# Optimization experiments

Hardware: AMD Instinct MI355X
Metric: run time of the kernel (lower is better)

## Reference

```python
import jax, jax.numpy as jnp
import numpy as np

N_NODE = 100000
N_EDGE = 1600000
D_FEAT = 64
DEPTH = 3
BASEALPHA = 1.0


def setup_inputs() -> dict:
    key = jax.random.key(0)
    k1, k2, k3 = jax.random.split(key, 3)
    x = jax.random.normal(k1, (N_NODE, D_FEAT), dtype=jnp.float32)
    edge_index = jax.random.randint(k2, (2, N_EDGE), 0, N_NODE, dtype=jnp.int64)
    edge_attr = jax.random.uniform(k3, (N_EDGE,), dtype=jnp.float32)
    # learnable polynomial coefficients, init = min(1/alpha, 1) = 1.0
    alphas = jnp.ones((DEPTH + 1,), dtype=jnp.float32)
    return {"x": x, "edge_index": edge_index, "edge_attr": edge_attr, "alphas": alphas}


def reference(x, edge_index, edge_attr, alphas):
    n = x.shape[0]
    row, col = edge_index[0], edge_index[1]
    # GCN symmetric degree normalization: val_e = d_row^-1/2 * w_e * d_col^-1/2
    deg = jax.ops.segment_sum(edge_attr, row, num_segments=n)
    safe_deg = jnp.where(deg > 0, deg, 1.0)
    dinv = jnp.where(deg > 0, jax.lax.rsqrt(safe_deg), 0.0)
    val = dinv[row] * edge_attr * dinv[col]  # [E]

    a = BASEALPHA * jnp.tanh(alphas)  # [depth+1]

    def spmm(h):  # (adj @ h): out[i] = sum_{e: row_e=i} val_e * h[col_e]
        return jax.ops.segment_sum(val[:, None] * h[col], row, num_segments=n)

    # PowerConv recurrence: x_0 = x; x_L = a_L * (adj @ x_{L-1})
    xs = [x]
    for L in range(1, DEPTH + 1):
        xs.append(a[L] * spmm(xs[-1]))
    return jnp.stack(xs, axis=1)  # [N, depth+1, d]
```

## Files before the change

### kernel.cpp

```cpp
#include <hip/hip_runtime.h>
#include <math.h>

#define N_NODE 100000
#define N_EDGE 1600000
#define D_FEAT 64
#define DEPTH  3
#define OUT_STRIDE ((DEPTH + 1) * D_FEAT)

#define NB  256
#define RPB 391
#define CAP 8192
#define S1_BS 512
#define S1_CHUNK 8192
#define S1_BLOCKS ((N_EDGE + S1_CHUNK - 1) / S1_CHUNK)

#define DEG_SCALE 33554432.0f

__device__ __forceinline__ unsigned int bf16_rne(float f) {
    unsigned int u = __float_as_uint(f);
    return (u + 0x7FFFu + ((u >> 16) & 1u)) >> 16;
}

__global__ __launch_bounds__(S1_BS) void stage1_bucket(
        const int* __restrict__ ei, const float* __restrict__ ea,
        int* __restrict__ bucket_cursor, int2* __restrict__ bucket) {
    __shared__ int hist[NB];
    __shared__ int segb[NB];
    int tid = threadIdx.x;
    int e0 = blockIdx.x * S1_CHUNK;

    for (int i = tid; i < NB; i += S1_BS) hist[i] = 0;
    __syncthreads();

    for (int k = 0; k < S1_CHUNK; k += S1_BS) {
        int e = e0 + k + tid;
        if (e < N_EDGE) {
            int r = ei[e];
            atomicAdd(&hist[r / RPB], 1);
        }
    }
    __syncthreads();

    for (int i = tid; i < NB; i += S1_BS) {
        int h = hist[i];
        segb[i] = (h > 0) ? atomicAdd(&bucket_cursor[i], h) : 0;
        hist[i] = 0;
    }
    __syncthreads();

    for (int k = 0; k < S1_CHUNK; k += S1_BS) {
        int e = e0 + k + tid;
        if (e < N_EDGE) {
            int r  = ei[e];
            int b  = r / RPB;
            int rl = r - b * RPB;
            int c  = ei[N_EDGE + e];
            float w = ea[e];
            int lofs = atomicAdd(&hist[b], 1);
            int pos  = segb[b] + lofs;
            if (pos < CAP)
                bucket[(size_t)b * CAP + pos] =
                    make_int2((rl << 17) | c, __float_as_int(w));
        }
    }
}

__global__ void bucket_scan_kernel(const int* __restrict__ bucket_cursor,
                                   int* __restrict__ bucket_base,
                                   const float* __restrict__ alphas,
                                   float* __restrict__ a_vals) {
    __shared__ int sc[NB];
    int tid = threadIdx.x;
    int v = bucket_cursor[tid];
    sc[tid] = v;
    __syncthreads();
    for (int off = 1; off < NB; off <<= 1) {
        int t = (tid >= off) ? sc[tid - off] : 0;
        __syncthreads();
        sc[tid] += t;
        __syncthreads();
    }
    bucket_base[tid] = sc[tid] - v;
    if (tid < DEPTH + 1) a_vals[tid] = tanhf(alphas[tid]);
}

__global__ __launch_bounds__(1024) void stage2_fused(
        const int2* __restrict__ bucket, const int* __restrict__ bucket_cnt,
        const int* __restrict__ bucket_base,
        int* __restrict__ row_ptr, int* __restrict__ row_end,
        float* __restrict__ dinv, int2* __restrict__ csr) {
    __shared__ int          rcnt[RPB];
    __shared__ unsigned int wdeg[RPB];
    __shared__ int          sc[512];
    __shared__ int          lcur[RPB];
    __shared__ int2         staged[CAP];
    int b = blockIdx.x, tid = threadIdx.x;

    for (int i = tid; i < RPB; i += 1024) { rcnt[i] = 0; wdeg[i] = 0u; }
    __syncthreads();

    int cnt = bucket_cnt[b];
    const int2* src = bucket + (size_t)b * CAP;
    for (int i = tid; i < cnt; i += 1024) {
        int2 e = src[i];
        int rl = e.x >> 17;
        float w = __int_as_float(e.y);
        atomicAdd(&rcnt[rl], 1);
        atomicAdd(&wdeg[rl], (unsigned int)(w * DEG_SCALE + 0.5f));
    }
    __syncthreads();

    int v = 0;
    if (tid < 512) { v = (tid < RPB) ? rcnt[tid] : 0; sc[tid] = v; }
    __syncthreads();
    for (int off = 1; off < 512; off <<= 1) {
        int t = 0;
        if (tid < 512 && tid >= off) t = sc[tid - off];
        __syncthreads();
        if (tid < 512) sc[tid] += t;
        __syncthreads();
    }

    int base_b = bucket_base[b];
    if (tid < RPB) {
        int excl = sc[tid] - v;
        lcur[tid] = excl;
        int row = b * RPB + tid;
        if (row < N_NODE) {
            row_ptr[row] = base_b + excl;
            row_end[row] = base_b + excl + rcnt[tid];
            float d = (float)wdeg[tid] * (1.0f / DEG_SCALE);
            dinv[row] = (d > 0.0f) ? rsqrtf(d) : 0.0f;
        }
    }
    __syncthreads();

    for (int i = tid; i < cnt; i += 1024) {
        int2 e = src[i];
        int rl = e.x >> 17;
        int c  = e.x & 0x1FFFF;
        int pos = atomicAdd(&lcur[rl], 1);
        staged[pos] = make_int2(c, e.y);
    }
    __syncthreads();

    for (int i = tid; i < cnt; i += 1024) csr[base_b + i] = staged[i];
}

__global__ void init_out_kernel(const float* __restrict__ x,
                                const float* __restrict__ dinv,
                                float* __restrict__ out,
                                unsigned short* __restrict__ hb0,
                                int write_hb) {
    int i = blockIdx.x * blockDim.x + threadIdx.x;
    if (i < N_NODE * (D_FEAT / 4)) {
        int n  = i >> 4;
        int d4 = (i & 15) << 2;
        float4 v = *(const float4*)&x[(size_t)n * D_FEAT + d4];
        *(float4*)&out[(size_t)n * OUT_STRIDE + d4] = v;
        if (write_hb) {
            float s = dinv[n];
            uint2 o;
            o.x = bf16_rne(v.x * s) | (bf16_rne(v.y * s) << 16);
            o.y = bf16_rne(v.z * s) | (bf16_rne(v.w * s) << 16);
            *(uint2*)&hb0[(size_t)n * D_FEAT + d4] = o;
        }
    }
}

__global__ void spmm_bf16_kernel(const int* __restrict__ row_ptr,
                                 const int* __restrict__ row_end,
                                 const int2* __restrict__ csr,
                                 const float* __restrict__ a_vals,
                                 const float* __restrict__ dinv,
                                 const unsigned short* __restrict__ hsrc,
                                 unsigned short* __restrict__ hdst,
                                 float* __restrict__ out,
                                 int L, int write_hdst) {
    int node = blockIdx.x * (blockDim.x >> 6) + (threadIdx.x >> 6);
    int lane = threadIdx.x & 63;
    if (node >= N_NODE) return;
    int beg = row_ptr[node];
    int end = row_end[node];
    int g = lane >> 3;
    int q = lane & 7;

    float acc[8] = {0, 0, 0, 0, 0, 0, 0, 0};

    for (int chunk = beg; chunk < end; chunk += 64) {
        int idx = chunk + lane;
        int2 pv = (idx < end) ? csr[idx] : make_int2(0, 0);
        int navail = end - chunk;
        if (navail > 64) navail = 64;
        for (int t = 0; t < navail; t += 8) {
            int sub = t + g;
            int   cc = __shfl(pv.x, sub);
            float vv = __int_as_float(__shfl(pv.y, sub));
            bool valid = (sub < navail);
            int   c_safe = valid ? cc : 0;
            float v_safe = valid ? vv : 0.0f;
            uint4 hv = *(const uint4*)&hsrc[(size_t)c_safe * D_FEAT + (q << 3)];
            acc[0] += v_safe * __uint_as_float((hv.x & 0xFFFFu) << 16);
            acc[1] += v_safe * __uint_as_float(hv.x & 0xFFFF0000u);
            acc[2] += v_safe * __uint_as_float((hv.y & 0xFFFFu) << 16);
            acc[3] += v_safe * __uint_as_float(hv.y & 0xFFFF0000u);
            acc[4] += v_safe * __uint_as_float((hv.z & 0xFFFFu) << 16);
            acc[5] += v_safe * __uint_as_float(hv.z & 0xFFFF0000u);
            acc[6] += v_safe * __uint_as_float((hv.w & 0xFFFFu) << 16);
            acc[7] += v_safe * __uint_as_float(hv.w & 0xFFFF0000u);
        }
    }

    #pragma unroll
    for (int j = 0; j < 8; ++j) {
        acc[j] += __shfl_down(acc[j], 32);
        acc[j] += __shfl_down(acc[j], 16);
        acc[j] += __shfl_down(acc[j], 8);
    }

    if (g == 0) {
        float di = dinv[node];
        float aL = a_vals[L];
        float s1 = aL * di;
        float s2 = s1 * di;
        float4 r0 = make_float4(s1 * acc[0], s1 * acc[1],
                                s1 * acc[2], s1 * acc[3]);
        float4 r1 = make_float4(s1 * acc[4], s1 * acc[5],
                                s1 * acc[6], s1 * acc[7]);
        size_t ob = (size_t)node * OUT_STRIDE + L * D_FEAT + (q << 3);
        *(float4*)&out[ob]     = r0;
        *(float4*)&out[ob + 4] = r1;
        if (write_hdst) {
            uint4 o;
            o.x = bf16_rne(s2 * acc[0]) | (bf16_rne(s2 * acc[1]) << 16);
            o.y = bf16_rne(s2 * acc[2]) | (bf16_rne(s2 * acc[3]) << 16);
            o.z = bf16_rne(s2 * acc[4]) | (bf16_rne(s2 * acc[5]) << 16);
            o.w = bf16_rne(s2 * acc[6]) | (bf16_rne(s2 * acc[7]) << 16);
            *(uint4*)&hdst[(size_t)node * D_FEAT + (q << 3)] = o;
        }
    }
}

__global__ void spmm_f32_kernel(const int* __restrict__ row_ptr,
                                const int* __restrict__ row_end,
                                const int2* __restrict__ csr,
                                const float* __restrict__ a_vals,
                                const float* __restrict__ dinv,
                                float* __restrict__ out,
                                int L) {
    int node = blockIdx.x * (blockDim.x >> 6) + (threadIdx.x >> 6);
    int lane = threadIdx.x & 63;
    if (node >= N_NODE) return;
    int beg = row_ptr[node];
    int end = row_end[node];
    int g = lane >> 4;
    int q = lane & 15;
    int src_base = (L - 1) * D_FEAT + (q << 2);

    float4 acc = make_float4(0.0f, 0.0f, 0.0f, 0.0f);
    for (int chunk = beg; chunk < end; chunk += 64) {
        int idx = chunk + lane;
        int2 pv = (idx < end) ? csr[idx] : make_int2(0, 0);
        int navail = end - chunk;
        if (navail > 64) navail = 64;
        for (int t = 0; t < navail; t += 4) {
            int sub = t + g;
            int   cc = __shfl(pv.x, sub);
            float vv = __int_as_float(__shfl(pv.y, sub));
            bool valid = (sub < navail);
            int   c_safe = valid ? cc : 0;
            float v_safe = valid ? (vv * dinv[c_safe]) : 0.0f;
            const float4 hv =
                *(const float4*)&out[(size_t)c_safe * OUT_STRIDE + src_base];
            acc.x += v_safe * hv.x;
            acc.y += v_safe * hv.y;
            acc.z += v_safe * hv.z;
            acc.w += v_safe * hv.w;
        }
    }
    acc.x += __shfl_down(acc.x, 32);
    acc.y += __shfl_down(acc.y, 32);
    acc.z += __shfl_down(acc.z, 32);
    acc.w += __shfl_down(acc.w, 32);
    acc.x += __shfl_down(acc.x, 16);
    acc.y += __shfl_down(acc.y, 16);
    acc.z += __shfl_down(acc.z, 16);
    acc.w += __shfl_down(acc.w, 16);
    if (g == 0) {
        float s1 = a_vals[L] * dinv[node];
        float4 r = make_float4(s1 * acc.x, s1 * acc.y, s1 * acc.z, s1 * acc.w);
        *(float4*)&out[(size_t)node * OUT_STRIDE + L * D_FEAT + (q << 2)] = r;
    }
}

extern "C" void kernel_launch(void* const* d_in, const int* in_sizes, int n_in,
                              void* d_out, int out_size, void* d_ws, size_t ws_size,
                              hipStream_t stream) {
    const float* x      = (const float*)d_in[0];
    const int*   ei     = (const int*)d_in[1];
    const float* ea     = (const float*)d_in[2];
    const float* alphas = (const float*)d_in[3];
    float*       out    = (float*)d_out;

    int2*  csr          = (int2*)d_ws;
    int*   row_ptr      = (int*)(csr + N_EDGE);
    int*   row_end      = row_ptr + N_NODE;
    float* dinv         = (float*)(row_end + N_NODE);
    int*   bucket_cursor= (int*)(dinv + N_NODE);
    int*   bucket_base  = bucket_cursor + NB;
    float* a_vals       = (float*)(bucket_base + NB);
    int2*  bucket       = (int2*)(a_vals + 4);
    unsigned short* hb0 = (unsigned short*)bucket;
    unsigned short* hb1 = hb0 + (size_t)N_NODE * D_FEAT;

    size_t base_bytes = (size_t)((char*)bucket - (char*)d_ws);
    size_t need_bf16  = base_bytes +
        2 * (size_t)N_NODE * D_FEAT * sizeof(unsigned short);
    int use_bf16 = (ws_size >= need_bf16) ? 1 : 0;

    hipMemsetAsync(bucket_cursor, 0, NB * sizeof(int), stream);

    stage1_bucket<<<S1_BLOCKS, S1_BS, 0, stream>>>(ei, ea, bucket_cursor, bucket);
    bucket_scan_kernel<<<1, NB, 0, stream>>>(bucket_cursor, bucket_base,
                                             alphas, a_vals);
    stage2_fused<<<NB, 1024, 0, stream>>>(bucket, bucket_cursor, bucket_base,
                                          row_ptr, row_end, dinv, csr);
    init_out_kernel<<<(N_NODE * (D_FEAT / 4) + 255) / 256, 256, 0, stream>>>(
        x, dinv, out, hb0, use_bf16);

    int nodes_per_block = 256 / 64;
    int spmm_blocks = (N_NODE + nodes_per_block - 1) / nodes_per_block;
    if (use_bf16) {
        spmm_bf16_kernel<<<spmm_blocks, 256, 0, stream>>>(row_ptr, row_end, csr,
            a_vals, dinv, hb0, hb1, out, 1, 1);
        spmm_bf16_kernel<<<spmm_blocks, 256, 0, stream>>>(row_ptr, row_end, csr,
            a_vals, dinv, hb1, hb0, out, 2, 1);
        spmm_bf16_kernel<<<spmm_blocks, 256, 0, stream>>>(row_ptr, row_end, csr,
            a_vals, dinv, hb0, hb1, out, 3, 0);
    } else {
        for (int L = 1; L <= DEPTH; ++L) {
            spmm_f32_kernel<<<spmm_blocks, 256, 0, stream>>>(row_ptr, row_end, csr,
                a_vals, dinv, out, L);
        }
    }
}
```

Baseline: 331.2 us.

## Split bf16 feature buffers into 16-feature slabs processed in separate passes

Stores the bf16 hidden features as four contiguous slabs of 16 features each and runs each SpMM as four passes, one per slab, so each pass gathers from a 3.2MB slab that fits in cache. Each wavefront now handles 32 edges at a time with 2 lanes per edge, which adds two more shuffle reduction steps. The edge list is therefore read four times per layer, and it is loaded with nontemporal loads. Output stores are also made nontemporal.

```diff
diff --git a/kernel.cpp b/kernel.cpp
--- a/kernel.cpp
+++ b/kernel.cpp
@@ -14,7 +14,14 @@
 #define S1_CHUNK 8192
 #define S1_BLOCKS ((N_EDGE + S1_CHUNK - 1) / S1_CHUNK)
 
+#define PASSES 4
+#define FPP    16
+#define NODES_PER_BLOCK 4
+#define BPP (N_NODE / NODES_PER_BLOCK)
+
 #define DEG_SCALE 33554432.0f
+
+typedef float  f32x4 __attribute__((ext_vector_type(4)));
 
 __device__ __forceinline__ unsigned int bf16_rne(float f) {
     unsigned int u = __float_as_uint(f);
@@ -157,49 +164,62 @@
         int n  = i >> 4;
         int d4 = (i & 15) << 2;
         float4 v = *(const float4*)&x[(size_t)n * D_FEAT + d4];
-        *(float4*)&out[(size_t)n * OUT_STRIDE + d4] = v;
+        f32x4 vv = {v.x, v.y, v.z, v.w};
+        __builtin_nontemporal_store(
+            vv, (f32x4*)&out[(size_t)n * OUT_STRIDE + d4]);
         if (write_hb) {
             float s = dinv[n];
+            int pass = d4 >> 4;
+            int fo   = d4 & 15;
             uint2 o;
             o.x = bf16_rne(v.x * s) | (bf16_rne(v.y * s) << 16);
             o.y = bf16_rne(v.z * s) | (bf16_rne(v.w * s) << 16);
-            *(uint2*)&hb0[(size_t)n * D_FEAT + d4] = o;
-        }
-    }
-}
-
-__global__ void spmm_bf16_kernel(const int* __restrict__ row_ptr,
-                                 const int* __restrict__ row_end,
-                                 const int2* __restrict__ csr,
-                                 const float* __restrict__ a_vals,
-                                 const float* __restrict__ dinv,
-                                 const unsigned short* __restrict__ hsrc,
-                                 unsigned short* __restrict__ hdst,
-                                 float* __restrict__ out,
-                                 int L, int write_hdst) {
-    int node = blockIdx.x * (blockDim.x >> 6) + (threadIdx.x >> 6);
+            *(uint2*)&hb0[((size_t)pass * N_NODE + n) * FPP + fo] = o;
+        }
+    }
+}
+
+__global__ __launch_bounds__(256) void spmm_bf16_kernel(
+        const int* __restrict__ row_ptr,
+        const int* __restrict__ row_end,
+        const int2* __restrict__ csr,
+        const float* __restrict__ a_vals,
+        const float* __restrict__ dinv,
+        const unsigned short* __restrict__ hsrc,
+        unsigned short* __restrict__ hdst,
+        float* __restrict__ out,
+        int L, int write_hdst) {
+    int pass = blockIdx.x / BPP;
+    int nb   = blockIdx.x - pass * BPP;
+    int node = nb * NODES_PER_BLOCK + (threadIdx.x >> 6);
     int lane = threadIdx.x & 63;
-    if (node >= N_NODE) return;
     int beg = row_ptr[node];
     int end = row_end[node];
-    int g = lane >> 3;
-    int q = lane & 7;
+    int s = lane >> 1;
+    int f = lane & 1;
+
+    const unsigned short* slab = hsrc + (size_t)pass * N_NODE * FPP;
 
     float acc[8] = {0, 0, 0, 0, 0, 0, 0, 0};
 
     for (int chunk = beg; chunk < end; chunk += 64) {
         int idx = chunk + lane;
-        int2 pv = (idx < end) ? csr[idx] : make_int2(0, 0);
+        int2 pv = make_int2(0, 0);
+        if (idx < end) {
+            long long t =
+                __builtin_nontemporal_load((const long long*)(csr + idx));
+            pv = *(int2*)&t;
+        }
         int navail = end - chunk;
         if (navail > 64) navail = 64;
-        for (int t = 0; t < navail; t += 8) {
-            int sub = t + g;
+        for (int t = 0; t < navail; t += 32) {
+            int sub = t + s;
             int   cc = __shfl(pv.x, sub);
             float vv = __int_as_float(__shfl(pv.y, sub));
             bool valid = (sub < navail);
             int   c_safe = valid ? cc : 0;
             float v_safe = valid ? vv : 0.0f;
-            uint4 hv = *(const uint4*)&hsrc[(size_t)c_safe * D_FEAT + (q << 3)];
+            uint4 hv = *(const uint4*)&slab[(size_t)c_safe * FPP + (f << 3)];
             acc[0] += v_safe * __uint_as_float((hv.x & 0xFFFFu) << 16);
             acc[1] += v_safe * __uint_as_float(hv.x & 0xFFFF0000u);
             acc[2] += v_safe * __uint_as_float((hv.y & 0xFFFFu) << 16);
@@ -216,27 +236,28 @@
         acc[j] += __shfl_down(acc[j], 32);
         acc[j] += __shfl_down(acc[j], 16);
         acc[j] += __shfl_down(acc[j], 8);
-    }
-
-    if (g == 0) {
+        acc[j] += __shfl_down(acc[j], 4);
+        acc[j] += __shfl_down(acc[j], 2);
+    }
+
+    if (lane < 2) {
         float di = dinv[node];
         float aL = a_vals[L];
         float s1 = aL * di;
         float s2 = s1 * di;
-        float4 r0 = make_float4(s1 * acc[0], s1 * acc[1],
-                                s1 * acc[2], s1 * acc[3]);
-        float4 r1 = make_float4(s1 * acc[4], s1 * acc[5],
-                                s1 * acc[6], s1 * acc[7]);
-        size_t ob = (size_t)node * OUT_STRIDE + L * D_FEAT + (q << 3);
-        *(float4*)&out[ob]     = r0;
-        *(float4*)&out[ob + 4] = r1;
+        f32x4 r0 = {s1 * acc[0], s1 * acc[1], s1 * acc[2], s1 * acc[3]};
+        f32x4 r1 = {s1 * acc[4], s1 * acc[5], s1 * acc[6], s1 * acc[7]};
+        size_t ob = (size_t)node * OUT_STRIDE + L * D_FEAT + pass * FPP
+                  + (lane << 3);
+        __builtin_nontemporal_store(r0, (f32x4*)&out[ob]);
+        __builtin_nontemporal_store(r1, (f32x4*)&out[ob + 4]);
         if (write_hdst) {
             uint4 o;
             o.x = bf16_rne(s2 * acc[0]) | (bf16_rne(s2 * acc[1]) << 16);
             o.y = bf16_rne(s2 * acc[2]) | (bf16_rne(s2 * acc[3]) << 16);
             o.z = bf16_rne(s2 * acc[4]) | (bf16_rne(s2 * acc[5]) << 16);
             o.w = bf16_rne(s2 * acc[6]) | (bf16_rne(s2 * acc[7]) << 16);
-            *(uint4*)&hdst[(size_t)node * D_FEAT + (q << 3)] = o;
+            *(uint4*)&hdst[((size_t)pass * N_NODE + node) * FPP + (lane << 3)] = o;
         }
     }
 }
@@ -328,16 +349,17 @@
     init_out_kernel<<<(N_NODE * (D_FEAT / 4) + 255) / 256, 256, 0, stream>>>(
         x, dinv, out, hb0, use_bf16);
 
-    int nodes_per_block = 256 / 64;
-    int spmm_blocks = (N_NODE + nodes_per_block - 1) / nodes_per_block;
     if (use_bf16) {
-        spmm_bf16_kernel<<<spmm_blocks, 256, 0, stream>>>(row_ptr, row_end, csr,
+        int grid = PASSES * BPP;
+        spmm_bf16_kernel<<<grid, 256, 0, stream>>>(row_ptr, row_end, csr,
             a_vals, dinv, hb0, hb1, out, 1, 1);
-        spmm_bf16_kernel<<<spmm_blocks, 256, 0, stream>>>(row_ptr, row_end, csr,
+        spmm_bf16_kernel<<<grid, 256, 0, stream>>>(row_ptr, row_end, csr,
             a_vals, dinv, hb1, hb0, out, 2, 1);
-        spmm_bf16_kernel<<<spmm_blocks, 256, 0, stream>>>(row_ptr, row_end, csr,
+        spmm_bf16_kernel<<<grid, 256, 0, stream>>>(row_ptr, row_end, csr,
             a_vals, dinv, hb0, hb1, out, 3, 0);
     } else {
+        int nodes_per_block = 256 / 64;
+        int spmm_blocks = (N_NODE + nodes_per_block - 1) / nodes_per_block;
         for (int L = 1; L <= DEPTH; ++L) {
             spmm_f32_kernel<<<spmm_blocks, 256, 0, stream>>>(row_ptr, row_end, csr,
                 a_vals, dinv, out, L);
```

Result: slower. 696.8 us (+110.4%).

## Sub-sort CSR rows by column octant and use nontemporal output stores

Applied to the files above, without the earlier changes.

The CSR build now counting-sorts edges within each row by column range (16 octants of node ids), so SpMM gathers of h[col] walk memory in a more ordered way and get better cache locality. The prefix scan is widened to cover row×octant cells. Output writes to the large result tensor use nontemporal stores so they do not evict the gather working set from cache. A launch bound of 256 is added to the bf16 SpMM kernel. The extra per-edge divide and the larger scan add work to CSR construction.

```diff
diff --git a/kernel.cpp b/kernel.cpp
--- a/kernel.cpp
+++ b/kernel.cpp
@@ -14,7 +14,14 @@
 #define S1_CHUNK 8192
 #define S1_BLOCKS ((N_EDGE + S1_CHUNK - 1) / S1_CHUNK)
 
+#define NOCT 16
+#define OCT_DIV 6250
+#define NCELL (RPB * NOCT)
+#define NCHUNK (NCELL / 8)
+
 #define DEG_SCALE 33554432.0f
+
+typedef float  f32x4 __attribute__((ext_vector_type(4)));
 
 __device__ __forceinline__ unsigned int bf16_rne(float f) {
     unsigned int u = __float_as_uint(f);
@@ -89,57 +96,76 @@
         const int* __restrict__ bucket_base,
         int* __restrict__ row_ptr, int* __restrict__ row_end,
         float* __restrict__ dinv, int2* __restrict__ csr) {
-    __shared__ int          rcnt[RPB];
+    __shared__ int          cnt2[NCELL];
     __shared__ unsigned int wdeg[RPB];
-    __shared__ int          sc[512];
-    __shared__ int          lcur[RPB];
+    __shared__ int          sc[1024];
     __shared__ int2         staged[CAP];
     int b = blockIdx.x, tid = threadIdx.x;
 
-    for (int i = tid; i < RPB; i += 1024) { rcnt[i] = 0; wdeg[i] = 0u; }
+    for (int i = tid; i < NCELL; i += 1024) cnt2[i] = 0;
+    if (tid < RPB) wdeg[tid] = 0u;
     __syncthreads();
 
     int cnt = bucket_cnt[b];
     const int2* src = bucket + (size_t)b * CAP;
-    for (int i = tid; i < cnt; i += 1024) {
-        int2 e = src[i];
-        int rl = e.x >> 17;
-        float w = __int_as_float(e.y);
-        atomicAdd(&rcnt[rl], 1);
-        atomicAdd(&wdeg[rl], (unsigned int)(w * DEG_SCALE + 0.5f));
-    }
-    __syncthreads();
-
-    int v = 0;
-    if (tid < 512) { v = (tid < RPB) ? rcnt[tid] : 0; sc[tid] = v; }
-    __syncthreads();
-    for (int off = 1; off < 512; off <<= 1) {
-        int t = 0;
-        if (tid < 512 && tid >= off) t = sc[tid - off];
-        __syncthreads();
-        if (tid < 512) sc[tid] += t;
-        __syncthreads();
-    }
-
-    int base_b = bucket_base[b];
-    if (tid < RPB) {
-        int excl = sc[tid] - v;
-        lcur[tid] = excl;
-        int row = b * RPB + tid;
-        if (row < N_NODE) {
-            row_ptr[row] = base_b + excl;
-            row_end[row] = base_b + excl + rcnt[tid];
-            float d = (float)wdeg[tid] * (1.0f / DEG_SCALE);
-            dinv[row] = (d > 0.0f) ? rsqrtf(d) : 0.0f;
-        }
-    }
-    __syncthreads();
 
     for (int i = tid; i < cnt; i += 1024) {
         int2 e = src[i];
         int rl = e.x >> 17;
         int c  = e.x & 0x1FFFF;
-        int pos = atomicAdd(&lcur[rl], 1);
+        int oc = c / OCT_DIV;
+        atomicAdd(&cnt2[rl * NOCT + oc], 1);
+        atomicAdd(&wdeg[rl],
+                  (unsigned int)(__int_as_float(e.y) * DEG_SCALE + 0.5f));
+    }
+    __syncthreads();
+
+    int lsum = 0;
+    if (tid < NCHUNK) {
+        int base = tid * 8;
+        #pragma unroll
+        for (int j = 0; j < 8; ++j) lsum += cnt2[base + j];
+    }
+    sc[tid] = lsum;
+    __syncthreads();
+    for (int off = 1; off < 1024; off <<= 1) {
+        int t = (tid >= off) ? sc[tid - off] : 0;
+        __syncthreads();
+        sc[tid] += t;
+        __syncthreads();
+    }
+    if (tid < NCHUNK) {
+        int run = sc[tid] - lsum;
+        int base = tid * 8;
+        #pragma unroll
+        for (int j = 0; j < 8; ++j) {
+            int v = cnt2[base + j];
+            cnt2[base + j] = run;
+            run += v;
+        }
+    }
+    __syncthreads();
+
+    int base_b = bucket_base[b];
+    if (tid < RPB) {
+        int row = b * RPB + tid;
+        if (row < N_NODE) {
+            int rb = cnt2[tid * NOCT];
+            int re = (tid == RPB - 1) ? cnt : cnt2[(tid + 1) * NOCT];
+            row_ptr[row] = base_b + rb;
+            row_end[row] = base_b + re;
+            float d = (float)wdeg[tid] * (1.0f / DEG_SCALE);
+            dinv[row] = (d > 0.0f) ? rsqrtf(d) : 0.0f;
+        }
+    }
+    __syncthreads();
+
+    for (int i = tid; i < cnt; i += 1024) {
+        int2 e = src[i];
+        int rl = e.x >> 17;
+        int c  = e.x & 0x1FFFF;
+        int oc = c / OCT_DIV;
+        int pos = atomicAdd(&cnt2[rl * NOCT + oc], 1);
         staged[pos] = make_int2(c, e.y);
     }
     __syncthreads();
@@ -157,7 +183,9 @@
         int n  = i >> 4;
         int d4 = (i & 15) << 2;
         float4 v = *(const float4*)&x[(size_t)n * D_FEAT + d4];
-        *(float4*)&out[(size_t)n * OUT_STRIDE + d4] = v;
+        f32x4 vv = {v.x, v.y, v.z, v.w};
+        __builtin_nontemporal_store(
+            vv, (f32x4*)&out[(size_t)n * OUT_STRIDE + d4]);
         if (write_hb) {
             float s = dinv[n];
             uint2 o;
@@ -168,15 +196,16 @@
     }
 }
 
-__global__ void spmm_bf16_kernel(const int* __restrict__ row_ptr,
-                                 const int* __restrict__ row_end,
-                                 const int2* __restrict__ csr,
-                                 const float* __restrict__ a_vals,
-                                 const float* __restrict__ dinv,
-                                 const unsigned short* __restrict__ hsrc,
-                                 unsigned short* __restrict__ hdst,
-                                 float* __restrict__ out,
-                                 int L, int write_hdst) {
+__global__ __launch_bounds__(256) void spmm_bf16_kernel(
+        const int* __restrict__ row_ptr,
+        const int* __restrict__ row_end,
+        const int2* __restrict__ csr,
+        const float* __restrict__ a_vals,
+        const float* __restrict__ dinv,
+        const unsigned short* __restrict__ hsrc,
+        unsigned short* __restrict__ hdst,
+        float* __restrict__ out,
+        int L, int write_hdst) {
     int node = blockIdx.x * (blockDim.x >> 6) + (threadIdx.x >> 6);
     int lane = threadIdx.x & 63;
     if (node >= N_NODE) return;
@@ -223,13 +252,11 @@
         float aL = a_vals[L];
         float s1 = aL * di;
         float s2 = s1 * di;
-        float4 r0 = make_float4(s1 * acc[0], s1 * acc[1],
-                                s1 * acc[2], s1 * acc[3]);
-        float4 r1 = make_float4(s1 * acc[4], s1 * acc[5],
-                                s1 * acc[6], s1 * acc[7]);
+        f32x4 r0 = {s1 * acc[0], s1 * acc[1], s1 * acc[2], s1 * acc[3]};
+        f32x4 r1 = {s1 * acc[4], s1 * acc[5], s1 * acc[6], s1 * acc[7]};
         size_t ob = (size_t)node * OUT_STRIDE + L * D_FEAT + (q << 3);
-        *(float4*)&out[ob]     = r0;
-        *(float4*)&out[ob + 4] = r1;
+        __builtin_nontemporal_store(r0, (f32x4*)&out[ob]);
+        __builtin_nontemporal_store(r1, (f32x4*)&out[ob + 4]);
         if (write_hdst) {
             uint4 o;
             o.x = bf16_rne(s2 * acc[0]) | (bf16_rne(s2 * acc[1]) << 16);
```

After: 331.3 us. Within noise of the previous version (+0.0%).
